# Kernel optimization log

Hardware: AMD Instinct MI355X
Metric: run time of the kernel (lower is better)

## Reference

```python
import jax, jax.numpy as jnp
import numpy as np

B, N, G = 32, 1024, 8   # batch, Nvecs (= k_in), Nglobals
K_OUT, H = 128, 128     # MLP output width, hidden width
D_IN = 1 + N + G        # MLP input width: [u, norm, dots]


def setup_inputs() -> dict:
    key = jax.random.key(0)
    ks = jax.random.split(key, 8)
    x = jax.random.uniform(ks[0], (B, N, 3), dtype=jnp.float32)  # positive coords -> dots >= 0
    u = jax.random.normal(ks[1], (B, G), dtype=jnp.float32)
    s0 = 1.0 / np.sqrt(D_IN)
    s1 = 1.0 / np.sqrt(H)
    W0 = jax.random.normal(ks[2], (D_IN, H), dtype=jnp.float32) * s0
    b0 = jnp.zeros((H,), dtype=jnp.float32)
    W1 = jax.random.normal(ks[3], (H, H), dtype=jnp.float32) * s1
    b1 = jnp.zeros((H,), dtype=jnp.float32)
    W2 = jax.random.normal(ks[4], (H, K_OUT), dtype=jnp.float32) * s1
    b2 = jnp.zeros((K_OUT,), dtype=jnp.float32)
    return {"x": x, "u": u, "W0": W0, "b0": b0, "W1": W1, "b1": b1, "W2": W2, "b2": b2}


def reference(x, u, W0, b0, W1, b1, W2, b2):
    # x: [B, N, 3], u: [B, G]
    norms = jnp.linalg.norm(x, axis=-1, keepdims=True)            # [B, N, 1]
    dots = jnp.sqrt(jnp.einsum('bid,bjd->bij', x, x))             # [B, N, N]
    u_rep = jnp.broadcast_to(u[:, None, :], (x.shape[0], x.shape[1], u.shape[-1]))
    scalars = jnp.concatenate([u_rep, norms, dots], axis=-1)      # [B, N, G+1+N]
    # MLP (Linear -> LeakyReLU -> Linear -> LeakyReLU -> Linear)
    h = jax.nn.leaky_relu(scalars @ W0 + b0)
    h = jax.nn.leaky_relu(h @ W1 + b1)
    fk = h @ W2 + b2                                              # [B, N, K_OUT]
    # outer product 'bio,bid->biod' followed by mean over i == fused contraction
    out = jnp.einsum('bio,bid->bod', fk, x) / x.shape[1]          # [B, K_OUT, 3]
    return out
```

## Files before the change

kernel.cpp:

```cpp
#include <hip/hip_runtime.h>
#include <hip/hip_fp16.h>

typedef _Float16 f16;
typedef f16 f16x4 __attribute__((ext_vector_type(4)));
typedef f16 f16x8 __attribute__((ext_vector_type(8)));
typedef float f32x4 __attribute__((ext_vector_type(4)));

#define NN 1024

#define IMG2_OFF  0
#define W8_OFF    327680
#define BIAS0_OFF 328192

__global__ __launch_bounds__(256) void prep_kernel(
    const float* __restrict__ u,  const float* __restrict__ W0,
    const float* __restrict__ b0, const float* __restrict__ W1,
    const float* __restrict__ W2,
    f16* __restrict__ img2, float* __restrict__ w8v, float* __restrict__ bias0,
    float* __restrict__ outp)
{
    const int t = threadIdx.x;
    const int blk = blockIdx.x;
    if (blk < 160) {
        int flat = blk * 1024 + t * 4;
        int c   = flat >> 13;
        int rem = flat & 8191;
        int s0  = rem & 7;
        int lm  = (rem >> 3) & 15;
        int q   = (rem >> 7) & 3;
        int ks  = (rem >> 9) & 1;
        int nt  = (rem >> 10) & 3;
        int wn  = (rem >> 12) & 1;
        int n = wn * 64 + nt * 16 + lm;
        f16x4 v;
#pragma unroll
        for (int e = 0; e < 4; ++e) {
            int k = ks * 32 + q * 8 + s0 + e;
            float val;
            if (c < 16)       val = W0[(9 + c * 64 + k) * 128 + n];
            else if (c < 18)  val = W1[((c - 16) * 64 + k) * 128 + n];
            else              val = W2[((c - 18) * 64 + k) * 128 + n];
            v[e] = (f16)val;
        }
        *(f16x4*)&img2[flat] = v;
    } else if (blk < 176) {
        int idx = (blk - 160) * 256 + t;
        int b = idx >> 7, h = idx & 127;
        float s = b0[h];
#pragma unroll
        for (int g = 0; g < 8; ++g) s += u[b * 8 + g] * W0[g * 128 + h];
        bias0[idx] = s;
    } else if (blk == 176) {
        if (t < 128) w8v[t] = W0[8 * 128 + t];
    } else {
        int idx = (blk - 177) * 1024 + t * 4;
        if (idx < 12288) { float4 z = {0.f, 0.f, 0.f, 0.f}; *(float4*)&outp[idx] = z; }
    }
}

__global__ __launch_bounds__(256, 2) void fused_kernel(
    const float* __restrict__ x, const float* __restrict__ b1p,
    const float* __restrict__ b2p, const f16* __restrict__ img2,
    const float* __restrict__ w8v, const float* __restrict__ bias0,
    float* __restrict__ outp)
{
    __shared__ __align__(16) f16 Dsh[2][64 * 64];
    __shared__ __align__(16) f16 xjsh[1024 * 4];
    __shared__ __align__(16) float xi[64 * 4];
    __shared__ float normv[64];
    __shared__ float biass[128];
    __shared__ float w8s[128];

    const int t = threadIdx.x;
    const int b = blockIdx.x >> 4;
    const int i0 = (blockIdx.x & 15) * 64;

    const int lane = t & 63, wv = t >> 6;
    const int lm = lane & 15, q = lane >> 4;
    const int half = wv >> 1;
    const int nbase = (wv & 1) * 2;
    f16* Hh = &Dsh[0][0];

    {
        const float* xb = x + (size_t)b * NN * 3;
        float4 v0 = *(const float4*)(xb + t * 12);
        float4 v1 = *(const float4*)(xb + t * 12 + 4);
        float4 v2 = *(const float4*)(xb + t * 12 + 8);
        f16x4 r0; r0[0] = (f16)v0.x; r0[1] = (f16)v0.y; r0[2] = (f16)v0.z; r0[3] = (f16)0;
        f16x4 r1; r1[0] = (f16)v0.w; r1[1] = (f16)v1.x; r1[2] = (f16)v1.y; r1[3] = (f16)0;
        f16x4 r2; r2[0] = (f16)v1.z; r2[1] = (f16)v1.w; r2[2] = (f16)v2.x; r2[3] = (f16)0;
        f16x4 r3; r3[0] = (f16)v2.y; r3[1] = (f16)v2.z; r3[2] = (f16)v2.w; r3[3] = (f16)0;
        *(f16x4*)&xjsh[(t * 4 + 0) * 4] = r0;
        *(f16x4*)&xjsh[(t * 4 + 1) * 4] = r1;
        *(f16x4*)&xjsh[(t * 4 + 2) * 4] = r2;
        *(f16x4*)&xjsh[(t * 4 + 3) * 4] = r3;
    }
    if (t < 192) {
        int i = t / 3, d = t - i * 3;
        xi[i * 4 + d] = x[(size_t)(b * NN + i0 + i) * 3 + d];
    }
    if (t < 128) { biass[t] = bias0[b * 128 + t]; w8s[t] = w8v[t]; }
    __syncthreads();
    if (t < 64) {
        float a0 = xi[t * 4], a1 = xi[t * 4 + 1], a2 = xi[t * 4 + 2];
        normv[t] = __builtin_amdgcn_sqrtf(a0 * a0 + a1 * a1 + a2 * a2);
    }

    f16x4 bi[4];
#pragma unroll
    for (int it = 0; it < 4; ++it) {
        f16x4 v; v[0] = (f16)0; v[1] = (f16)0; v[2] = (f16)0; v[3] = (f16)0;
        if (q == 0) {
            int ii = it * 16 + lm;
            v[0] = (f16)xi[ii * 4];
            v[1] = (f16)xi[ii * 4 + 1];
            v[2] = (f16)xi[ii * 4 + 2];
        }
        bi[it] = v;
    }

    auto dotstore = [&](int jc, int buf) {
        f16x4 ajv; ajv[0] = (f16)0; ajv[1] = (f16)0; ajv[2] = (f16)0; ajv[3] = (f16)0;
        if (q == 0)
            ajv = *(const f16x4*)&xjsh[(jc * 64 + wv * 16 + lm) * 4];
#pragma unroll
        for (int it = 0; it < 4; ++it) {
            f32x4 z; z[0] = 0.f; z[1] = 0.f; z[2] = 0.f; z[3] = 0.f;
            f32x4 cg = __builtin_amdgcn_mfma_f32_16x16x16f16(ajv, bi[it], z, 0, 0, 0);
            f16x4 dv;
#pragma unroll
            for (int r = 0; r < 4; ++r)
                dv[r] = (f16)__builtin_amdgcn_sqrtf(fmaxf(cg[r], 0.f));
            int row = it * 16 + lm;
            int colstart = wv * 16 + q * 4;
            int addr = row * 64 + (((colstart & ~7) ^ ((row & 7) << 3)) | (colstart & 7));
            *(f16x4*)&Dsh[buf][addr] = dv;
        }
    };

    f32x4 acc[4][2];
    auto zero_acc = [&]() {
#pragma unroll
        for (int mt = 0; mt < 4; ++mt)
#pragma unroll
            for (int n2 = 0; n2 < 2; ++n2)
#pragma unroll
                for (int e = 0; e < 4; ++e) acc[mt][n2][e] = 0.f;
    };
    zero_acc();

    f16x8 bfbuf[2][2][2];
    {
        const f16* wb = img2 + (size_t)(0 * 2 + half) * 4096 + lane * 8;
#pragma unroll
        for (int n2 = 0; n2 < 2; ++n2)
#pragma unroll
            for (int ks = 0; ks < 2; ++ks)
                bfbuf[0][n2][ks] = *(const f16x8*)(wb + (((nbase + n2) * 2 + ks)) * 512);
    }
    dotstore(0, 0);
    __syncthreads();

#pragma unroll
    for (int jc = 0; jc < 16; ++jc) {
        const int cur = jc & 1, nxt = cur ^ 1;
        if (jc < 15) {
            const f16* wb = img2 + (size_t)((jc + 1) * 2 + half) * 4096 + lane * 8;
#pragma unroll
            for (int n2 = 0; n2 < 2; ++n2)
#pragma unroll
                for (int ks = 0; ks < 2; ++ks)
                    bfbuf[nxt][n2][ks] = *(const f16x8*)(wb + (((nbase + n2) * 2 + ks)) * 512);
        }
        f16x8 af[4][2];
#pragma unroll
        for (int mt = 0; mt < 4; ++mt)
#pragma unroll
            for (int ks = 0; ks < 2; ++ks) {
                int row = mt * 16 + lm;
                int col = ks * 32 + q * 8;
                af[mt][ks] = *(const f16x8*)(Dsh[cur] + row * 64 + (col ^ ((row & 7) << 3)));
            }
        if (jc < 15) dotstore(jc + 1, nxt);
#pragma unroll
        for (int ks = 0; ks < 2; ++ks)
#pragma unroll
            for (int mt = 0; mt < 4; ++mt)
#pragma unroll
                for (int n2 = 0; n2 < 2; ++n2)
                    acc[mt][n2] = __builtin_amdgcn_mfma_f32_16x16x32_f16(
                        af[mt][ks], bfbuf[cur][n2][ks], acc[mt][n2], 0, 0, 0);
        __syncthreads();
    }

    f16x8 bL[2][4];
#pragma unroll
    for (int n2 = 0; n2 < 2; ++n2)
#pragma unroll
        for (int ks = 0; ks < 4; ++ks) {
            const f16* wb = img2 + (size_t)((16 + (ks >> 1)) * 2 + half) * 4096 + lane * 8;
            bL[n2][ks] = *(const f16x8*)(wb + (((nbase + n2) * 2 + (ks & 1))) * 512);
        }

#pragma unroll
    for (int mt = 0; mt < 4; ++mt)
#pragma unroll
        for (int n2 = 0; n2 < 2; ++n2) {
            const int h = wv * 32 + n2 * 16 + lm;
            const float bh = biass[h], w8h = w8s[h];
#pragma unroll
            for (int r = 0; r < 4; ++r) {
                int i = mt * 16 + q * 4 + r;
                float val = acc[mt][n2][r] + bh + normv[i] * w8h;
                val = val > 0.f ? val : 0.01f * val;
                int addr = i * 128 + (((h & ~7) ^ ((i & 7) << 3)) | (h & 7));
                Hh[addr] = (f16)val;
            }
        }
    __syncthreads();

    zero_acc();
    {
        f16x8 af[4][4];
#pragma unroll
        for (int mt = 0; mt < 4; ++mt)
#pragma unroll
            for (int ks = 0; ks < 4; ++ks) {
                int row = mt * 16 + lm;
                int col = ks * 32 + q * 8;
                af[mt][ks] = *(const f16x8*)(Hh + row * 128 + (col ^ ((row & 7) << 3)));
            }
#pragma unroll
        for (int ks = 0; ks < 4; ++ks)
#pragma unroll
            for (int mt = 0; mt < 4; ++mt)
#pragma unroll
                for (int n2 = 0; n2 < 2; ++n2)
                    acc[mt][n2] = __builtin_amdgcn_mfma_f32_16x16x32_f16(
                        af[mt][ks], bL[n2][ks], acc[mt][n2], 0, 0, 0);
    }

    f16x8 bM[2][4];
#pragma unroll
    for (int n2 = 0; n2 < 2; ++n2)
#pragma unroll
        for (int ks = 0; ks < 4; ++ks) {
            const f16* wb = img2 + (size_t)((18 + (ks >> 1)) * 2 + half) * 4096 + lane * 8;
            bM[n2][ks] = *(const f16x8*)(wb + (((nbase + n2) * 2 + (ks & 1))) * 512);
        }
    __syncthreads();

#pragma unroll
    for (int mt = 0; mt < 4; ++mt)
#pragma unroll
        for (int n2 = 0; n2 < 2; ++n2) {
            const int h = wv * 32 + n2 * 16 + lm;
            const float bh = b1p[h];
#pragma unroll
            for (int r = 0; r < 4; ++r) {
                int i = mt * 16 + q * 4 + r;
                float val = acc[mt][n2][r] + bh;
                val = val > 0.f ? val : 0.01f * val;
                int addr = i * 128 + (((h & ~7) ^ ((i & 7) << 3)) | (h & 7));
                Hh[addr] = (f16)val;
            }
        }
    __syncthreads();

    zero_acc();
    {
        f16x8 af[4][4];
#pragma unroll
        for (int mt = 0; mt < 4; ++mt)
#pragma unroll
            for (int ks = 0; ks < 4; ++ks) {
                int row = mt * 16 + lm;
                int col = ks * 32 + q * 8;
                af[mt][ks] = *(const f16x8*)(Hh + row * 128 + (col ^ ((row & 7) << 3)));
            }
#pragma unroll
        for (int ks = 0; ks < 4; ++ks)
#pragma unroll
            for (int mt = 0; mt < 4; ++mt)
#pragma unroll
                for (int n2 = 0; n2 < 2; ++n2)
                    acc[mt][n2] = __builtin_amdgcn_mfma_f32_16x16x32_f16(
                        af[mt][ks], bM[n2][ks], acc[mt][n2], 0, 0, 0);
    }

    float p[2][3];
#pragma unroll
    for (int n2 = 0; n2 < 2; ++n2)
#pragma unroll
        for (int d = 0; d < 3; ++d) p[n2][d] = 0.f;
    float bo[2];
#pragma unroll
    for (int n2 = 0; n2 < 2; ++n2) bo[n2] = b2p[wv * 32 + n2 * 16 + lm];
#pragma unroll
    for (int mt = 0; mt < 4; ++mt)
#pragma unroll
        for (int r = 0; r < 4; ++r) {
            int i = mt * 16 + q * 4 + r;
            float x0 = xi[i * 4], x1 = xi[i * 4 + 1], x2 = xi[i * 4 + 2];
#pragma unroll
            for (int n2 = 0; n2 < 2; ++n2) {
                float fkv = acc[mt][n2][r] + bo[n2];
                p[n2][0] = fmaf(fkv, x0, p[n2][0]);
                p[n2][1] = fmaf(fkv, x1, p[n2][1]);
                p[n2][2] = fmaf(fkv, x2, p[n2][2]);
            }
        }
#pragma unroll
    for (int n2 = 0; n2 < 2; ++n2)
#pragma unroll
        for (int d = 0; d < 3; ++d) {
            float s = p[n2][d];
            s += __shfl_xor(s, 16);
            s += __shfl_xor(s, 32);
            if (q == 0) {
                int o = wv * 32 + n2 * 16 + lm;
                atomicAdd(&outp[(b * 128 + o) * 3 + d], s * (1.0f / 1024.0f));
            }
        }
}

extern "C" void kernel_launch(void* const* d_in, const int* in_sizes, int n_in,
                              void* d_out, int out_size, void* d_ws, size_t ws_size,
                              hipStream_t stream) {
    const float* x  = (const float*)d_in[0];
    const float* u  = (const float*)d_in[1];
    const float* W0 = (const float*)d_in[2];
    const float* b0 = (const float*)d_in[3];
    const float* W1 = (const float*)d_in[4];
    const float* b1 = (const float*)d_in[5];
    const float* W2 = (const float*)d_in[6];
    const float* b2 = (const float*)d_in[7];

    char* ws = (char*)d_ws;
    f16*   img2  = (f16*)(ws + IMG2_OFF);
    float* w8v   = (float*)(ws + W8_OFF);
    float* bias0 = (float*)(ws + BIAS0_OFF);
    float* out   = (float*)d_out;

    prep_kernel<<<189, 256, 0, stream>>>(u, W0, b0, W1, W2, img2, w8v, bias0, out);
    fused_kernel<<<512, 256, 0, stream>>>(x, b1, b2, img2, w8v, bias0, out);
}
```

Baseline: 85.44 us.

## Split fused kernel work across eight waves per block instead of four

Doubles the block size to 512 threads so each wave owns a single 16-column N tile instead of two. The distance-tile generation is split across the i-halves and j-groups of the waves. Per-wave accumulators and B-fragment registers are halved, which aims at higher occupancy and more latency hiding. The cost is that each wave re-reads the full A fragments from LDS, so LDS traffic per MFMA doubles, and barriers now span more waves.

```diff
diff --git a/kernel.cpp b/kernel.cpp
--- a/kernel.cpp
+++ b/kernel.cpp
@@ -58,7 +58,7 @@
     }
 }
 
-__global__ __launch_bounds__(256, 2) void fused_kernel(
+__global__ __launch_bounds__(512, 4) void fused_kernel(
     const float* __restrict__ x, const float* __restrict__ b1p,
     const float* __restrict__ b2p, const f16* __restrict__ img2,
     const float* __restrict__ w8v, const float* __restrict__ bias0,
@@ -77,11 +77,13 @@
 
     const int lane = t & 63, wv = t >> 6;
     const int lm = lane & 15, q = lane >> 4;
-    const int half = wv >> 1;
-    const int nbase = (wv & 1) * 2;
+    const int half = wv >> 2;
+    const int ntw  = wv & 3;
+    const int jg   = wv & 3;
+    const int ih   = wv >> 2;
     f16* Hh = &Dsh[0][0];
 
-    {
+    if (t < 256) {
         const float* xb = x + (size_t)b * NN * 3;
         float4 v0 = *(const float4*)(xb + t * 12);
         float4 v1 = *(const float4*)(xb + t * 12 + 4);
@@ -94,69 +96,66 @@
         *(f16x4*)&xjsh[(t * 4 + 1) * 4] = r1;
         *(f16x4*)&xjsh[(t * 4 + 2) * 4] = r2;
         *(f16x4*)&xjsh[(t * 4 + 3) * 4] = r3;
-    }
-    if (t < 192) {
-        int i = t / 3, d = t - i * 3;
+    } else if (t < 448) {
+        int u2 = t - 256;
+        int i = u2 / 3, d = u2 - i * 3;
         xi[i * 4 + d] = x[(size_t)(b * NN + i0 + i) * 3 + d];
-    }
-    if (t < 128) { biass[t] = bias0[b * 128 + t]; w8s[t] = w8v[t]; }
+    } else {
+    }
+    if (t >= 256 && t < 384) { int h = t - 256; biass[h] = bias0[b * 128 + h]; w8s[h] = w8v[h]; }
     __syncthreads();
     if (t < 64) {
         float a0 = xi[t * 4], a1 = xi[t * 4 + 1], a2 = xi[t * 4 + 2];
         normv[t] = __builtin_amdgcn_sqrtf(a0 * a0 + a1 * a1 + a2 * a2);
     }
 
-    f16x4 bi[4];
-#pragma unroll
-    for (int it = 0; it < 4; ++it) {
+    f16x4 bi[2];
+#pragma unroll
+    for (int itl = 0; itl < 2; ++itl) {
         f16x4 v; v[0] = (f16)0; v[1] = (f16)0; v[2] = (f16)0; v[3] = (f16)0;
         if (q == 0) {
-            int ii = it * 16 + lm;
+            int ii = (ih * 2 + itl) * 16 + lm;
             v[0] = (f16)xi[ii * 4];
             v[1] = (f16)xi[ii * 4 + 1];
             v[2] = (f16)xi[ii * 4 + 2];
         }
-        bi[it] = v;
+        bi[itl] = v;
     }
 
     auto dotstore = [&](int jc, int buf) {
         f16x4 ajv; ajv[0] = (f16)0; ajv[1] = (f16)0; ajv[2] = (f16)0; ajv[3] = (f16)0;
         if (q == 0)
-            ajv = *(const f16x4*)&xjsh[(jc * 64 + wv * 16 + lm) * 4];
-#pragma unroll
-        for (int it = 0; it < 4; ++it) {
+            ajv = *(const f16x4*)&xjsh[(jc * 64 + jg * 16 + lm) * 4];
+#pragma unroll
+        for (int itl = 0; itl < 2; ++itl) {
             f32x4 z; z[0] = 0.f; z[1] = 0.f; z[2] = 0.f; z[3] = 0.f;
-            f32x4 cg = __builtin_amdgcn_mfma_f32_16x16x16f16(ajv, bi[it], z, 0, 0, 0);
+            f32x4 cg = __builtin_amdgcn_mfma_f32_16x16x16f16(ajv, bi[itl], z, 0, 0, 0);
             f16x4 dv;
 #pragma unroll
             for (int r = 0; r < 4; ++r)
                 dv[r] = (f16)__builtin_amdgcn_sqrtf(fmaxf(cg[r], 0.f));
-            int row = it * 16 + lm;
-            int colstart = wv * 16 + q * 4;
+            int row = (ih * 2 + itl) * 16 + lm;
+            int colstart = jg * 16 + q * 4;
             int addr = row * 64 + (((colstart & ~7) ^ ((row & 7) << 3)) | (colstart & 7));
             *(f16x4*)&Dsh[buf][addr] = dv;
         }
     };
 
-    f32x4 acc[4][2];
+    f32x4 acc[4];
     auto zero_acc = [&]() {
 #pragma unroll
         for (int mt = 0; mt < 4; ++mt)
 #pragma unroll
-            for (int n2 = 0; n2 < 2; ++n2)
-#pragma unroll
-                for (int e = 0; e < 4; ++e) acc[mt][n2][e] = 0.f;
+            for (int e = 0; e < 4; ++e) acc[mt][e] = 0.f;
     };
     zero_acc();
 
-    f16x8 bfbuf[2][2][2];
+    f16x8 bfbuf[2][2];
     {
         const f16* wb = img2 + (size_t)(0 * 2 + half) * 4096 + lane * 8;
 #pragma unroll
-        for (int n2 = 0; n2 < 2; ++n2)
-#pragma unroll
-            for (int ks = 0; ks < 2; ++ks)
-                bfbuf[0][n2][ks] = *(const f16x8*)(wb + (((nbase + n2) * 2 + ks)) * 512);
+        for (int ks = 0; ks < 2; ++ks)
+            bfbuf[0][ks] = *(const f16x8*)(wb + (ntw * 2 + ks) * 512);
     }
     dotstore(0, 0);
     __syncthreads();
@@ -167,10 +166,8 @@
         if (jc < 15) {
             const f16* wb = img2 + (size_t)((jc + 1) * 2 + half) * 4096 + lane * 8;
 #pragma unroll
-            for (int n2 = 0; n2 < 2; ++n2)
-#pragma unroll
-                for (int ks = 0; ks < 2; ++ks)
-                    bfbuf[nxt][n2][ks] = *(const f16x8*)(wb + (((nbase + n2) * 2 + ks)) * 512);
+            for (int ks = 0; ks < 2; ++ks)
+                bfbuf[nxt][ks] = *(const f16x8*)(wb + (ntw * 2 + ks) * 512);
         }
         f16x8 af[4][2];
 #pragma unroll
@@ -186,142 +183,109 @@
         for (int ks = 0; ks < 2; ++ks)
 #pragma unroll
             for (int mt = 0; mt < 4; ++mt)
-#pragma unroll
-                for (int n2 = 0; n2 < 2; ++n2)
-                    acc[mt][n2] = __builtin_amdgcn_mfma_f32_16x16x32_f16(
-                        af[mt][ks], bfbuf[cur][n2][ks], acc[mt][n2], 0, 0, 0);
+                acc[mt] = __builtin_amdgcn_mfma_f32_16x16x32_f16(
+                    af[mt][ks], bfbuf[cur][ks], acc[mt], 0, 0, 0);
         __syncthreads();
     }
 
-    f16x8 bL[2][4];
-#pragma unroll
-    for (int n2 = 0; n2 < 2; ++n2)
-#pragma unroll
-        for (int ks = 0; ks < 4; ++ks) {
-            const f16* wb = img2 + (size_t)((16 + (ks >> 1)) * 2 + half) * 4096 + lane * 8;
-            bL[n2][ks] = *(const f16x8*)(wb + (((nbase + n2) * 2 + (ks & 1))) * 512);
-        }
-
-#pragma unroll
-    for (int mt = 0; mt < 4; ++mt)
-#pragma unroll
-        for (int n2 = 0; n2 < 2; ++n2) {
-            const int h = wv * 32 + n2 * 16 + lm;
-            const float bh = biass[h], w8h = w8s[h];
-#pragma unroll
-            for (int r = 0; r < 4; ++r) {
-                int i = mt * 16 + q * 4 + r;
-                float val = acc[mt][n2][r] + bh + normv[i] * w8h;
-                val = val > 0.f ? val : 0.01f * val;
-                int addr = i * 128 + (((h & ~7) ^ ((i & 7) << 3)) | (h & 7));
-                Hh[addr] = (f16)val;
-            }
-        }
+    f16x8 bL[4];
+#pragma unroll
+    for (int ks = 0; ks < 4; ++ks) {
+        const f16* wb = img2 + (size_t)((16 + (ks >> 1)) * 2 + half) * 4096 + lane * 8;
+        bL[ks] = *(const f16x8*)(wb + (ntw * 2 + (ks & 1)) * 512);
+    }
+
+    const int hw = wv * 16 + lm;
+#pragma unroll
+    for (int mt = 0; mt < 4; ++mt) {
+        const float bh = biass[hw], w8h = w8s[hw];
+#pragma unroll
+        for (int r = 0; r < 4; ++r) {
+            int i = mt * 16 + q * 4 + r;
+            float val = acc[mt][r] + bh + normv[i] * w8h;
+            val = val > 0.f ? val : 0.01f * val;
+            int addr = i * 128 + (((hw & ~7) ^ ((i & 7) << 3)) | (hw & 7));
+            Hh[addr] = (f16)val;
+        }
+    }
     __syncthreads();
 
     zero_acc();
-    {
-        f16x8 af[4][4];
+#pragma unroll
+    for (int ks = 0; ks < 4; ++ks) {
+        f16x8 af[4];
+#pragma unroll
+        for (int mt = 0; mt < 4; ++mt) {
+            int row = mt * 16 + lm;
+            int col = ks * 32 + q * 8;
+            af[mt] = *(const f16x8*)(Hh + row * 128 + (col ^ ((row & 7) << 3)));
+        }
 #pragma unroll
         for (int mt = 0; mt < 4; ++mt)
-#pragma unroll
-            for (int ks = 0; ks < 4; ++ks) {
-                int row = mt * 16 + lm;
-                int col = ks * 32 + q * 8;
-                af[mt][ks] = *(const f16x8*)(Hh + row * 128 + (col ^ ((row & 7) << 3)));
-            }
-#pragma unroll
-        for (int ks = 0; ks < 4; ++ks)
-#pragma unroll
-            for (int mt = 0; mt < 4; ++mt)
-#pragma unroll
-                for (int n2 = 0; n2 < 2; ++n2)
-                    acc[mt][n2] = __builtin_amdgcn_mfma_f32_16x16x32_f16(
-                        af[mt][ks], bL[n2][ks], acc[mt][n2], 0, 0, 0);
-    }
-
-    f16x8 bM[2][4];
-#pragma unroll
-    for (int n2 = 0; n2 < 2; ++n2)
-#pragma unroll
-        for (int ks = 0; ks < 4; ++ks) {
-            const f16* wb = img2 + (size_t)((18 + (ks >> 1)) * 2 + half) * 4096 + lane * 8;
-            bM[n2][ks] = *(const f16x8*)(wb + (((nbase + n2) * 2 + (ks & 1))) * 512);
-        }
-    __syncthreads();
-
-#pragma unroll
-    for (int mt = 0; mt < 4; ++mt)
-#pragma unroll
-        for (int n2 = 0; n2 < 2; ++n2) {
-            const int h = wv * 32 + n2 * 16 + lm;
-            const float bh = b1p[h];
-#pragma unroll
-            for (int r = 0; r < 4; ++r) {
-                int i = mt * 16 + q * 4 + r;
-                float val = acc[mt][n2][r] + bh;
-                val = val > 0.f ? val : 0.01f * val;
-                int addr = i * 128 + (((h & ~7) ^ ((i & 7) << 3)) | (h & 7));
-                Hh[addr] = (f16)val;
-            }
-        }
+            acc[mt] = __builtin_amdgcn_mfma_f32_16x16x32_f16(
+                af[mt], bL[ks], acc[mt], 0, 0, 0);
+    }
+
+    f16x8 bM[4];
+#pragma unroll
+    for (int ks = 0; ks < 4; ++ks) {
+        const f16* wb = img2 + (size_t)((18 + (ks >> 1)) * 2 + half) * 4096 + lane * 8;
+        bM[ks] = *(const f16x8*)(wb + (ntw * 2 + (ks & 1)) * 512);
+    }
+    __syncthreads();
+
+#pragma unroll
+    for (int mt = 0; mt < 4; ++mt) {
+        const float bh = b1p[hw];
+#pragma unroll
+        for (int r = 0; r < 4; ++r) {
+            int i = mt * 16 + q * 4 + r;
+            float val = acc[mt][r] + bh;
+            val = val > 0.f ? val : 0.01f * val;
+            int addr = i * 128 + (((hw & ~7) ^ ((i & 7) << 3)) | (hw & 7));
+            Hh[addr] = (f16)val;
+        }
+    }
     __syncthreads();
 
     zero_acc();
-    {
-        f16x8 af[4][4];
+#pragma unroll
+    for (int ks = 0; ks < 4; ++ks) {
+        f16x8 af[4];
+#pragma unroll
+        for (int mt = 0; mt < 4; ++mt) {
+            int row = mt * 16 + lm;
+            int col = ks * 32 + q * 8;
+            af[mt] = *(const f16x8*)(Hh + row * 128 + (col ^ ((row & 7) << 3)));
+        }
 #pragma unroll
         for (int mt = 0; mt < 4; ++mt)
-#pragma unroll
-            for (int ks = 0; ks < 4; ++ks) {
-                int row = mt * 16 + lm;
-                int col = ks * 32 + q * 8;
-                af[mt][ks] = *(const f16x8*)(Hh + row * 128 + (col ^ ((row & 7) << 3)));
-            }
-#pragma unroll
-        for (int ks = 0; ks < 4; ++ks)
-#pragma unroll
-            for (int mt = 0; mt < 4; ++mt)
-#pragma unroll
-                for (int n2 = 0; n2 < 2; ++n2)
-                    acc[mt][n2] = __builtin_amdgcn_mfma_f32_16x16x32_f16(
-                        af[mt][ks], bM[n2][ks], acc[mt][n2], 0, 0, 0);
-    }
-
-    float p[2][3];
-#pragma unroll
-    for (int n2 = 0; n2 < 2; ++n2)
-#pragma unroll
-        for (int d = 0; d < 3; ++d) p[n2][d] = 0.f;
-    float bo[2];
-#pragma unroll
-    for (int n2 = 0; n2 < 2; ++n2) bo[n2] = b2p[wv * 32 + n2 * 16 + lm];
+            acc[mt] = __builtin_amdgcn_mfma_f32_16x16x32_f16(
+                af[mt], bM[ks], acc[mt], 0, 0, 0);
+    }
+
+    float p[3];
+    p[0] = 0.f; p[1] = 0.f; p[2] = 0.f;
+    const float bo = b2p[hw];
 #pragma unroll
     for (int mt = 0; mt < 4; ++mt)
 #pragma unroll
         for (int r = 0; r < 4; ++r) {
             int i = mt * 16 + q * 4 + r;
             float x0 = xi[i * 4], x1 = xi[i * 4 + 1], x2 = xi[i * 4 + 2];
-#pragma unroll
-            for (int n2 = 0; n2 < 2; ++n2) {
-                float fkv = acc[mt][n2][r] + bo[n2];
-                p[n2][0] = fmaf(fkv, x0, p[n2][0]);
-                p[n2][1] = fmaf(fkv, x1, p[n2][1]);
-                p[n2][2] = fmaf(fkv, x2, p[n2][2]);
-            }
-        }
-#pragma unroll
-    for (int n2 = 0; n2 < 2; ++n2)
-#pragma unroll
-        for (int d = 0; d < 3; ++d) {
-            float s = p[n2][d];
-            s += __shfl_xor(s, 16);
-            s += __shfl_xor(s, 32);
-            if (q == 0) {
-                int o = wv * 32 + n2 * 16 + lm;
-                atomicAdd(&outp[(b * 128 + o) * 3 + d], s * (1.0f / 1024.0f));
-            }
-        }
+            float fkv = acc[mt][r] + bo;
+            p[0] = fmaf(fkv, x0, p[0]);
+            p[1] = fmaf(fkv, x1, p[1]);
+            p[2] = fmaf(fkv, x2, p[2]);
+        }
+#pragma unroll
+    for (int d = 0; d < 3; ++d) {
+        float s = p[d];
+        s += __shfl_xor(s, 16);
+        s += __shfl_xor(s, 32);
+        if (q == 0)
+            atomicAdd(&outp[(b * 128 + hw) * 3 + d], s * (1.0f / 1024.0f));
+    }
 }
 
 extern "C" void kernel_launch(void* const* d_in, const int* in_sizes, int n_in,
@@ -343,5 +307,5 @@
     float* out   = (float*)d_out;
 
     prep_kernel<<<189, 256, 0, stream>>>(u, W0, b0, W1, W2, img2, w8v, bias0, out);
-    fused_kernel<<<512, 256, 0, stream>>>(x, b1, b2, img2, w8v, bias0, out);
+    fused_kernel<<<512, 512, 0, stream>>>(x, b1, b2, img2, w8v, bias0, out);
 }
```

Result: no change. 86.09 us (+0.8%).

## Double row tile to 128 per block with 512 threads sharing weight loads

Applied to the files above, without the earlier changes.

Each block now handles 128 rows of i instead of 64, using 8 waves split into two row halves that share the same W0/W1/W2 fragments and x_j staging. This halves the grid to 256 blocks and halves per-batch redundant loading of x into LDS and weight streaming per row. The layer-2/3 A-fragment loads are also restructured per k-step to reduce register pressure. Risks: fewer blocks (256 on 256 CUs) gives one block per CU and less latency hiding, and LDS use doubles.

```diff
diff --git a/kernel.cpp b/kernel.cpp
--- a/kernel.cpp
+++ b/kernel.cpp
@@ -58,30 +58,33 @@
     }
 }
 
-__global__ __launch_bounds__(256, 2) void fused_kernel(
+__global__ __launch_bounds__(512, 2) void fused_kernel(
     const float* __restrict__ x, const float* __restrict__ b1p,
     const float* __restrict__ b2p, const f16* __restrict__ img2,
     const float* __restrict__ w8v, const float* __restrict__ bias0,
     float* __restrict__ outp)
 {
-    __shared__ __align__(16) f16 Dsh[2][64 * 64];
+    __shared__ __align__(16) f16 Dsh[2][128 * 64];
     __shared__ __align__(16) f16 xjsh[1024 * 4];
-    __shared__ __align__(16) float xi[64 * 4];
-    __shared__ float normv[64];
+    __shared__ __align__(16) float xi[128 * 4];
+    __shared__ float normv[128];
     __shared__ float biass[128];
     __shared__ float w8s[128];
 
     const int t = threadIdx.x;
-    const int b = blockIdx.x >> 4;
-    const int i0 = (blockIdx.x & 15) * 64;
+    const int b = blockIdx.x >> 3;
+    const int i0 = (blockIdx.x & 7) * 128;
 
     const int lane = t & 63, wv = t >> 6;
     const int lm = lane & 15, q = lane >> 4;
-    const int half = wv >> 1;
-    const int nbase = (wv & 1) * 2;
+    const int ih = wv >> 2;
+    const int hq = wv & 3;
+    const int half = hq >> 1;
+    const int nbase = (hq & 1) * 2;
+    const int jg = wv & 3;
     f16* Hh = &Dsh[0][0];
 
-    {
+    if (t < 256) {
         const float* xb = x + (size_t)b * NN * 3;
         float4 v0 = *(const float4*)(xb + t * 12);
         float4 v1 = *(const float4*)(xb + t * 12 + 4);
@@ -94,14 +97,17 @@
         *(f16x4*)&xjsh[(t * 4 + 1) * 4] = r1;
         *(f16x4*)&xjsh[(t * 4 + 2) * 4] = r2;
         *(f16x4*)&xjsh[(t * 4 + 3) * 4] = r3;
-    }
-    if (t < 192) {
-        int i = t / 3, d = t - i * 3;
-        xi[i * 4 + d] = x[(size_t)(b * NN + i0 + i) * 3 + d];
-    }
-    if (t < 128) { biass[t] = bias0[b * 128 + t]; w8s[t] = w8v[t]; }
-    __syncthreads();
-    if (t < 64) {
+    } else {
+        int u2 = t - 256;
+        if (u2 < 128) { biass[u2] = bias0[b * 128 + u2]; w8s[u2] = w8v[u2]; }
+#pragma unroll
+        for (int e = u2; e < 384; e += 256) {
+            int i = e / 3, d = e - i * 3;
+            xi[i * 4 + d] = x[(size_t)(b * NN + i0 + i) * 3 + d];
+        }
+    }
+    __syncthreads();
+    if (t < 128) {
         float a0 = xi[t * 4], a1 = xi[t * 4 + 1], a2 = xi[t * 4 + 2];
         normv[t] = __builtin_amdgcn_sqrtf(a0 * a0 + a1 * a1 + a2 * a2);
     }
@@ -111,7 +117,7 @@
     for (int it = 0; it < 4; ++it) {
         f16x4 v; v[0] = (f16)0; v[1] = (f16)0; v[2] = (f16)0; v[3] = (f16)0;
         if (q == 0) {
-            int ii = it * 16 + lm;
+            int ii = ih * 64 + it * 16 + lm;
             v[0] = (f16)xi[ii * 4];
             v[1] = (f16)xi[ii * 4 + 1];
             v[2] = (f16)xi[ii * 4 + 2];
@@ -122,7 +128,7 @@
     auto dotstore = [&](int jc, int buf) {
         f16x4 ajv; ajv[0] = (f16)0; ajv[1] = (f16)0; ajv[2] = (f16)0; ajv[3] = (f16)0;
         if (q == 0)
-            ajv = *(const f16x4*)&xjsh[(jc * 64 + wv * 16 + lm) * 4];
+            ajv = *(const f16x4*)&xjsh[(jc * 64 + jg * 16 + lm) * 4];
 #pragma unroll
         for (int it = 0; it < 4; ++it) {
             f32x4 z; z[0] = 0.f; z[1] = 0.f; z[2] = 0.f; z[3] = 0.f;
@@ -131,8 +137,8 @@
 #pragma unroll
             for (int r = 0; r < 4; ++r)
                 dv[r] = (f16)__builtin_amdgcn_sqrtf(fmaxf(cg[r], 0.f));
-            int row = it * 16 + lm;
-            int colstart = wv * 16 + q * 4;
+            int row = ih * 64 + it * 16 + lm;
+            int colstart = jg * 16 + q * 4;
             int addr = row * 64 + (((colstart & ~7) ^ ((row & 7) << 3)) | (colstart & 7));
             *(f16x4*)&Dsh[buf][addr] = dv;
         }
@@ -156,7 +162,7 @@
         for (int n2 = 0; n2 < 2; ++n2)
 #pragma unroll
             for (int ks = 0; ks < 2; ++ks)
-                bfbuf[0][n2][ks] = *(const f16x8*)(wb + (((nbase + n2) * 2 + ks)) * 512);
+                bfbuf[0][n2][ks] = *(const f16x8*)(wb + ((nbase + n2) * 2 + ks) * 512);
     }
     dotstore(0, 0);
     __syncthreads();
@@ -170,14 +176,14 @@
             for (int n2 = 0; n2 < 2; ++n2)
 #pragma unroll
                 for (int ks = 0; ks < 2; ++ks)
-                    bfbuf[nxt][n2][ks] = *(const f16x8*)(wb + (((nbase + n2) * 2 + ks)) * 512);
+                    bfbuf[nxt][n2][ks] = *(const f16x8*)(wb + ((nbase + n2) * 2 + ks) * 512);
         }
         f16x8 af[4][2];
 #pragma unroll
         for (int mt = 0; mt < 4; ++mt)
 #pragma unroll
             for (int ks = 0; ks < 2; ++ks) {
-                int row = mt * 16 + lm;
+                int row = ih * 64 + mt * 16 + lm;
                 int col = ks * 32 + q * 8;
                 af[mt][ks] = *(const f16x8*)(Dsh[cur] + row * 64 + (col ^ ((row & 7) << 3)));
             }
@@ -199,18 +205,18 @@
 #pragma unroll
         for (int ks = 0; ks < 4; ++ks) {
             const f16* wb = img2 + (size_t)((16 + (ks >> 1)) * 2 + half) * 4096 + lane * 8;
-            bL[n2][ks] = *(const f16x8*)(wb + (((nbase + n2) * 2 + (ks & 1))) * 512);
+            bL[n2][ks] = *(const f16x8*)(wb + ((nbase + n2) * 2 + (ks & 1)) * 512);
         }
 
 #pragma unroll
     for (int mt = 0; mt < 4; ++mt)
 #pragma unroll
         for (int n2 = 0; n2 < 2; ++n2) {
-            const int h = wv * 32 + n2 * 16 + lm;
+            const int h = hq * 32 + n2 * 16 + lm;
             const float bh = biass[h], w8h = w8s[h];
 #pragma unroll
             for (int r = 0; r < 4; ++r) {
-                int i = mt * 16 + q * 4 + r;
+                int i = ih * 64 + mt * 16 + q * 4 + r;
                 float val = acc[mt][n2][r] + bh + normv[i] * w8h;
                 val = val > 0.f ? val : 0.01f * val;
                 int addr = i * 128 + (((h & ~7) ^ ((i & 7) << 3)) | (h & 7));
@@ -220,24 +226,21 @@
     __syncthreads();
 
     zero_acc();
-    {
-        f16x8 af[4][4];
+#pragma unroll
+    for (int ks = 0; ks < 4; ++ks) {
+        f16x8 af[4];
+#pragma unroll
+        for (int mt = 0; mt < 4; ++mt) {
+            int row = ih * 64 + mt * 16 + lm;
+            int col = ks * 32 + q * 8;
+            af[mt] = *(const f16x8*)(Hh + row * 128 + (col ^ ((row & 7) << 3)));
+        }
 #pragma unroll
         for (int mt = 0; mt < 4; ++mt)
 #pragma unroll
-            for (int ks = 0; ks < 4; ++ks) {
-                int row = mt * 16 + lm;
-                int col = ks * 32 + q * 8;
-                af[mt][ks] = *(const f16x8*)(Hh + row * 128 + (col ^ ((row & 7) << 3)));
-            }
-#pragma unroll
-        for (int ks = 0; ks < 4; ++ks)
-#pragma unroll
-            for (int mt = 0; mt < 4; ++mt)
-#pragma unroll
-                for (int n2 = 0; n2 < 2; ++n2)
-                    acc[mt][n2] = __builtin_amdgcn_mfma_f32_16x16x32_f16(
-                        af[mt][ks], bL[n2][ks], acc[mt][n2], 0, 0, 0);
+            for (int n2 = 0; n2 < 2; ++n2)
+                acc[mt][n2] = __builtin_amdgcn_mfma_f32_16x16x32_f16(
+                    af[mt], bL[n2][ks], acc[mt][n2], 0, 0, 0);
     }
 
     f16x8 bM[2][4];
@@ -246,7 +249,7 @@
 #pragma unroll
         for (int ks = 0; ks < 4; ++ks) {
             const f16* wb = img2 + (size_t)((18 + (ks >> 1)) * 2 + half) * 4096 + lane * 8;
-            bM[n2][ks] = *(const f16x8*)(wb + (((nbase + n2) * 2 + (ks & 1))) * 512);
+            bM[n2][ks] = *(const f16x8*)(wb + ((nbase + n2) * 2 + (ks & 1)) * 512);
         }
     __syncthreads();
 
@@ -254,11 +257,11 @@
     for (int mt = 0; mt < 4; ++mt)
 #pragma unroll
         for (int n2 = 0; n2 < 2; ++n2) {
-            const int h = wv * 32 + n2 * 16 + lm;
+            const int h = hq * 32 + n2 * 16 + lm;
             const float bh = b1p[h];
 #pragma unroll
             for (int r = 0; r < 4; ++r) {
-                int i = mt * 16 + q * 4 + r;
+                int i = ih * 64 + mt * 16 + q * 4 + r;
                 float val = acc[mt][n2][r] + bh;
                 val = val > 0.f ? val : 0.01f * val;
                 int addr = i * 128 + (((h & ~7) ^ ((i & 7) << 3)) | (h & 7));
@@ -268,24 +271,21 @@
     __syncthreads();
 
     zero_acc();
-    {
-        f16x8 af[4][4];
+#pragma unroll
+    for (int ks = 0; ks < 4; ++ks) {
+        f16x8 af[4];
+#pragma unroll
+        for (int mt = 0; mt < 4; ++mt) {
+            int row = ih * 64 + mt * 16 + lm;
+            int col = ks * 32 + q * 8;
+            af[mt] = *(const f16x8*)(Hh + row * 128 + (col ^ ((row & 7) << 3)));
+        }
 #pragma unroll
         for (int mt = 0; mt < 4; ++mt)
 #pragma unroll
-            for (int ks = 0; ks < 4; ++ks) {
-                int row = mt * 16 + lm;
-                int col = ks * 32 + q * 8;
-                af[mt][ks] = *(const f16x8*)(Hh + row * 128 + (col ^ ((row & 7) << 3)));
-            }
-#pragma unroll
-        for (int ks = 0; ks < 4; ++ks)
-#pragma unroll
-            for (int mt = 0; mt < 4; ++mt)
-#pragma unroll
-                for (int n2 = 0; n2 < 2; ++n2)
-                    acc[mt][n2] = __builtin_amdgcn_mfma_f32_16x16x32_f16(
-                        af[mt][ks], bM[n2][ks], acc[mt][n2], 0, 0, 0);
+            for (int n2 = 0; n2 < 2; ++n2)
+                acc[mt][n2] = __builtin_amdgcn_mfma_f32_16x16x32_f16(
+                    af[mt], bM[n2][ks], acc[mt][n2], 0, 0, 0);
     }
 
     float p[2][3];
@@ -295,12 +295,12 @@
         for (int d = 0; d < 3; ++d) p[n2][d] = 0.f;
     float bo[2];
 #pragma unroll
-    for (int n2 = 0; n2 < 2; ++n2) bo[n2] = b2p[wv * 32 + n2 * 16 + lm];
+    for (int n2 = 0; n2 < 2; ++n2) bo[n2] = b2p[hq * 32 + n2 * 16 + lm];
 #pragma unroll
     for (int mt = 0; mt < 4; ++mt)
 #pragma unroll
         for (int r = 0; r < 4; ++r) {
-            int i = mt * 16 + q * 4 + r;
+            int i = ih * 64 + mt * 16 + q * 4 + r;
             float x0 = xi[i * 4], x1 = xi[i * 4 + 1], x2 = xi[i * 4 + 2];
 #pragma unroll
             for (int n2 = 0; n2 < 2; ++n2) {
@@ -318,7 +318,7 @@
             s += __shfl_xor(s, 16);
             s += __shfl_xor(s, 32);
             if (q == 0) {
-                int o = wv * 32 + n2 * 16 + lm;
+                int o = hq * 32 + n2 * 16 + lm;
                 atomicAdd(&outp[(b * 128 + o) * 3 + d], s * (1.0f / 1024.0f));
             }
         }
@@ -343,5 +343,5 @@
     float* out   = (float*)d_out;
 
     prep_kernel<<<189, 256, 0, stream>>>(u, W0, b0, W1, W2, img2, w8v, bias0, out);
-    fused_kernel<<<512, 256, 0, stream>>>(x, b1, b2, img2, w8v, bias0, out);
+    fused_kernel<<<256, 512, 0, stream>>>(x, b1, b2, img2, w8v, bias0, out);
 }
```

Result: no change. 86.76 us (+1.5%).
